# Optimization experiments

Measured on AMD Instinct MI355X. Metric: run time of the kernel, lower is better.

The kernel has to match this reference:

```python
import jax, jax.numpy as jnp
import numpy as np

EPS = 1e-5

def _ln(x, g, b):
    mu = jnp.mean(x, axis=-1, keepdims=True)
    var = jnp.mean(jnp.square(x - mu), axis=-1, keepdims=True)
    return (x - mu) * jax.lax.rsqrt(var + EPS) * g + b

def setup_inputs() -> dict:
    B, T, D, E, H, M = 2, 2048, 1024, 8, 512, 2048
    key = jax.random.key(0)
    ks = jax.random.split(key, 24)
    s = 0.02
    inp = {}
    inp['x'] = jax.random.normal(ks[0], (B, T, D), jnp.float32)
    flat = jnp.arange(M, dtype=jnp.int32) * 2  # unique token ids over B*T
    inp['index_b'] = flat // T
    inp['index_t'] = flat % T
    # shared SwiGLU (hidden = H)
    inp['sw1'] = jax.random.normal(ks[1], (H, D), jnp.float32) * s
    inp['sb1'] = jnp.zeros((H,), jnp.float32)
    inp['sw2'] = jax.random.normal(ks[2], (H, D), jnp.float32) * s
    inp['sb2'] = jnp.zeros((H,), jnp.float32)
    inp['sw3'] = jax.random.normal(ks[3], (D, H), jnp.float32) * s
    inp['sb3'] = jnp.zeros((D,), jnp.float32)
    inp['s_ln_g'] = jnp.ones((H,), jnp.float32)
    inp['s_ln_b'] = jnp.zeros((H,), jnp.float32)
    # gates
    inp['sg_w'] = jax.random.normal(ks[4], (1, D), jnp.float32) * s
    inp['sg_b'] = jnp.zeros((1,), jnp.float32)
    inp['eg_w'] = jax.random.normal(ks[5], (E, D), jnp.float32) * s
    inp['eg_b'] = jnp.zeros((E,), jnp.float32)
    inp['exp_bias'] = jnp.zeros((E,), jnp.float32)
    # per-expert SwiGLU stacks
    inp['ew1'] = jax.random.normal(ks[6], (E, H, D), jnp.float32) * s
    inp['eb1'] = jnp.zeros((E, H), jnp.float32)
    inp['ew2'] = jax.random.normal(ks[7], (E, H, D), jnp.float32) * s
    inp['eb2'] = jnp.zeros((E, H), jnp.float32)
    inp['ew3'] = jax.random.normal(ks[8], (E, D, H), jnp.float32) * s
    inp['eb3'] = jnp.zeros((E, D), jnp.float32)
    inp['sel_ln_g'] = jnp.ones((H,), jnp.float32)
    inp['sel_ln_b'] = jnp.zeros((H,), jnp.float32)
    return inp

def _forward(x, index_b, index_t, sw1, sb1, sw2, sb2, sw3, sb3, s_ln_g, s_ln_b,
             sg_w, sg_b, eg_w, eg_b, exp_bias, ew1, eb1, ew2, eb2, ew3, eb3,
             sel_ln_g, sel_ln_b):
    # shared SwiGLU over all tokens: [B,T,D]
    x1 = jnp.einsum('btd,hd->bth', x, sw1) + sb1
    x2 = jnp.einsum('btd,hd->bth', x, sw2) + sb2
    sh = _ln(jax.nn.silu(x1) * x2, s_ln_g, s_ln_b)
    shared_out = jnp.einsum('bth,dh->btd', sh, sw3) + sb3
    # MoE tokens
    x_moe = x[index_b, index_t]  # [M,D]
    shared_scores = jax.nn.sigmoid(x_moe @ sg_w.T + sg_b)       # [M,1]
    expert_scores = jax.nn.sigmoid(x_moe @ eg_w.T + eg_b)       # [M,E]
    top1_idx = jnp.argmax(expert_scores + exp_bias, axis=-1)    # [M]
    top1_score = jnp.take_along_axis(expert_scores, top1_idx[:, None], axis=-1)  # [M,1]
    weights = jax.nn.softmax(jnp.concatenate([shared_scores, top1_score], axis=-1), axis=-1)
    shared_w, expert_w = weights[:, 0], weights[:, 1]
    shared_moe_out = shared_out[index_b, index_t] * shared_w[:, None]
    # per-expert SwiGLU computed densely for all E, then token selects its expert
    h1 = jnp.einsum('md,ehd->meh', x_moe, ew1) + eb1  # [M,E,H]
    h2 = jnp.einsum('md,ehd->meh', x_moe, ew2) + eb2
    z = _ln(jax.nn.silu(h1) * h2, sel_ln_g, sel_ln_b)
    out_all = jnp.einsum('meh,edh->med', z, ew3) + eb3  # [M,E,D]
    expert_out = jnp.take_along_axis(out_all, top1_idx[:, None, None], axis=1)[:, 0]  # [M,D]
    expert_moe_out = expert_out * expert_w[:, None]
    final_out = shared_out.at[index_b, index_t].set(shared_moe_out + expert_moe_out)
    return final_out

def reference(x, index_b, index_t, sw1, sb1, sw2, sb2, sw3, sb3, s_ln_g, s_ln_b,
              sg_w, sg_b, eg_w, eg_b, exp_bias, ew1, eb1, ew2, eb2, ew3, eb3,
              sel_ln_g, sel_ln_b):
    return _forward(x, index_b, index_t, sw1, sb1, sw2, sb2, sw3, sb3, s_ln_g, s_ln_b,
                    sg_w, sg_b, eg_w, eg_b, exp_bias, ew1, eb1, ew2, eb2, ew3, eb3,
                    sel_ln_g, sel_ln_b)
```

## Files before the change

### kernel.cpp

```cpp
#include <hip/hip_runtime.h>
#include <cstdint>

typedef unsigned short u16;
typedef __bf16 bf16x8 __attribute__((ext_vector_type(8)));
typedef float f32x4 __attribute__((ext_vector_type(4)));

#define T_SEQ  2048
#define D_DIM  1024
#define H_DIM  512
#define E_NUM  8
#define M_TOK  2048
#define BT_TOK 4096
#define MAXP   3072
#define NSPLIT_NONE (1 << 28)

static __device__ __forceinline__ u16 f2bf(float f) {
    union { float f; uint32_t u; } v; v.f = f;
    uint32_t u = v.u;
    return (u16)((u + 0x7FFFu + ((u >> 16) & 1u)) >> 16);
}
static __device__ __forceinline__ uint32_t pack2(float a, float b) {
    return (uint32_t)f2bf(a) | ((uint32_t)f2bf(b) << 16);
}

static __device__ __forceinline__ void gl_lds16(const u16* g, u16* l) {
    __builtin_amdgcn_global_load_lds(
        (const __attribute__((address_space(1))) uint32_t*)g,
        (__attribute__((address_space(3))) uint32_t*)l, 16, 0, 0);
}

static __device__ __forceinline__ int find_expert(int m, const int* __restrict__ base) {
    int e = 0;
    #pragma unroll
    for (int ee = 0; ee < E_NUM - 1; ++ee)
        if (m >= base[ee + 1]) e = ee + 1;
    return e;
}


__device__ __forceinline__ void gating_body(
    int m,
    const float* __restrict__ x,
    const int* __restrict__ ib, const int* __restrict__ itx,
    const float* __restrict__ sgw, const float* __restrict__ sgb,
    const float* __restrict__ egw, const float* __restrict__ egb,
    const float* __restrict__ ebias,
    float* __restrict__ shw, float* __restrict__ expw,
    int* __restrict__ top1, int* __restrict__ rowidx,
    float* xs, float* sc)
{
    int tid = threadIdx.x;
    int row = ib[m] * T_SEQ + itx[m];
    if (tid == 0) rowidx[m] = row;
    const float* xr = x + (size_t)row * D_DIM;
    ((float4*)xs)[tid] = ((const float4*)xr)[tid];
    __syncthreads();
    int lane = tid & 63, w4 = tid >> 6;
    for (int sidx = w4; sidx < 9; sidx += 4) {
        const float* wr = (sidx == 0) ? sgw : (egw + (size_t)(sidx - 1) * D_DIM);
        float acc = 0.f;
        #pragma unroll
        for (int i = 0; i < 4; ++i) {
            int idx = i * 64 + lane;
            float4 xv = ((const float4*)xs)[idx];
            float4 wv = ((const float4*)wr)[idx];
            acc += xv.x * wv.x + xv.y * wv.y + xv.z * wv.z + xv.w * wv.w;
        }
        #pragma unroll
        for (int o = 32; o > 0; o >>= 1) acc += __shfl_xor(acc, o);
        if (lane == 0) sc[sidx] = acc;
    }
    __syncthreads();
    if (tid == 0) {
        float ss = 1.f / (1.f + expf(-(sc[0] + sgb[0])));
        float es[E_NUM];
        float best = -1e30f; int bi = 0;
        #pragma unroll
        for (int e = 0; e < E_NUM; ++e) {
            es[e] = 1.f / (1.f + expf(-(sc[1 + e] + egb[e])));
            float t = es[e] + ebias[e];
            if (t > best) { best = t; bi = e; }
        }
        float ts = es[bi];
        shw[m]  = 1.f / (1.f + expf(ts - ss));
        expw[m] = 1.f / (1.f + expf(ss - ts));
        top1[m] = bi;
    }
}

__device__ __forceinline__ void bucket_body(
    const int* __restrict__ top1,
    int* __restrict__ base, int* __restrict__ cnt, int* __restrict__ perm,
    int* sm)
{
    int* lc  = sm;
    int* lb  = sm + E_NUM;
    int* cur = sm + 2 * E_NUM + 1;
    int tid = threadIdx.x;
    if (tid < E_NUM) { lc[tid] = 0; cur[tid] = 0; }
    __syncthreads();
    for (int m = tid; m < M_TOK; m += 256) atomicAdd(&lc[top1[m]], 1);
    __syncthreads();
    if (tid == 0) {
        int bacc = 0;
        for (int e = 0; e < E_NUM; ++e) { lb[e] = bacc; bacc += (lc[e] + 127) & ~127; }
        lb[E_NUM] = bacc;
    }
    __syncthreads();
    for (int m = tid; m < M_TOK; m += 256) {
        int e = top1[m];
        int pos = lb[e] + atomicAdd(&cur[e], 1);
        perm[pos] = m;
    }
    if (tid <= E_NUM) base[tid] = lb[tid];
    if (tid < E_NUM)  cnt[tid]  = lc[tid];
}

template<bool SEL>
__device__ __forceinline__ void ln_body(
    int m,
    const float* __restrict__ X,
    const float* __restrict__ g, const float* __restrict__ b,
    u16* __restrict__ out,
    const int* __restrict__ base, const int* __restrict__ cnt,
    float* red)
{
    int tid = threadIdx.x;
    if (SEL) {
        bool valid = false;
        int tot = base[E_NUM];
        if (m < tot) {
            int e = find_expert(m, base);
            valid = (m - base[e]) < cnt[e];
        }
        if (!valid) {
            out[(size_t)m * H_DIM + tid] = 0;
            out[(size_t)m * H_DIM + tid + 256] = 0;
            return;
        }
    }
    const float* row = X + (size_t)m * D_DIM;
    float a0 = row[tid],       c0 = row[H_DIM + tid];
    float a1 = row[tid + 256], c1 = row[H_DIM + tid + 256];
    float v0 = (a0 / (1.f + expf(-a0))) * c0;
    float v1 = (a1 / (1.f + expf(-a1))) * c1;
    float s = v0 + v1, s2 = v0 * v0 + v1 * v1;
    #pragma unroll
    for (int o = 32; o > 0; o >>= 1) {
        s  += __shfl_xor(s, o);
        s2 += __shfl_xor(s2, o);
    }
    int w = tid >> 6;
    if ((tid & 63) == 0) { red[w] = s; red[4 + w] = s2; }
    __syncthreads();
    s  = red[0] + red[1] + red[2] + red[3];
    s2 = red[4] + red[5] + red[6] + red[7];
    float mu  = s * (1.f / H_DIM);
    float var = s2 * (1.f / H_DIM) - mu * mu;
    float inv = rsqrtf(var + 1e-5f);
    out[(size_t)m * H_DIM + tid]       = f2bf((v0 - mu) * inv * g[tid] + b[tid]);
    out[(size_t)m * H_DIM + tid + 256] = f2bf((v1 - mu) * inv * g[tid + 256] + b[tid + 256]);
}

template<int MODE, int KLEN>
__device__ __forceinline__ void gemm_body(
    int bn, int bm,
    const u16* __restrict__ A, int lda,
    const u16* __restrict__ W0, const u16* __restrict__ W1, int nsplit,
    const float* __restrict__ b0, const float* __restrict__ b1,
    float* __restrict__ C,
    const int* __restrict__ base, const int* __restrict__ cnt,
    const int* __restrict__ perm, const int* __restrict__ rowidx,
    const float* __restrict__ shw, const float* __restrict__ expw,
    u16* lds)
{
    constexpr int NITER = KLEN / 64;
    const int tid   = threadIdx.x;
    const int mbase = bm * 128;

    int pend = 0;
    if (MODE >= 2) {
        const int tot = base[E_NUM];
        if (mbase >= tot) return;
        int e = find_expert(mbase, base);
        pend = base[e] + cnt[e];
        if (mbase >= pend) return;
        const size_t wstride = (size_t)H_DIM * D_DIM;
        W0 += (size_t)e * wstride;
        if (MODE == 2) W1 += (size_t)e * wstride;
        b0 += e * ((MODE == 2) ? H_DIM : D_DIM);
        if (MODE == 2) b1 += e * H_DIM;
    }

    const int w  = tid >> 6;
    const int l  = tid & 63;
    const int sr = tid >> 3;
    const int sc = tid & 7;

    const u16* agp[4];
    #pragma unroll
    for (int t = 0; t < 4; ++t) {
        int r = t * 32 + sr;
        int grow;
        if (MODE == 2) {
            int p  = mbase + r;
            int pp = (p < pend) ? p : (pend - 1);
            grow = rowidx[perm[pp]];
        } else {
            grow = mbase + r;
        }
        agp[t] = A + (size_t)grow * lda + (sc ^ (r & 7)) * 8;
    }
    const u16* bgp[4];
    #pragma unroll
    for (int t = 0; t < 4; ++t) {
        int r = t * 32 + sr;
        int n = bn * 128 + r;
        bgp[t] = ((n < nsplit) ? (W0 + (size_t)n * KLEN)
                               : (W1 + (size_t)(n - nsplit) * KLEN)) + (sc ^ (r & 7)) * 8;
    }

    const int l16 = l & 15, quad = l >> 4;
    const int wm = w >> 1, wn = w & 1;

    int avo[4], bvo[4];
    #pragma unroll
    for (int i = 0; i < 4; ++i) {
        int R = wm * 64 + i * 16 + l16;
        avo[i] = R * 128 + ((quad ^ (R & 7)) * 16);
    }
    #pragma unroll
    for (int j = 0; j < 4; ++j) {
        int R = wn * 64 + j * 16 + l16;
        bvo[j] = 16384 + R * 128 + ((quad ^ (R & 7)) * 16);
    }

    f32x4 acc[4][4];
    #pragma unroll
    for (int i = 0; i < 4; ++i)
        #pragma unroll
        for (int j = 0; j < 4; ++j)
            acc[i][j] = (f32x4){0.f, 0.f, 0.f, 0.f};

    const int kstart = (bm + bn * 3) & (NITER - 1);
    const char* ldsc = (const char*)lds;

    {
        int k0 = kstart * 64;
        #pragma unroll
        for (int t = 0; t < 4; ++t)
            gl_lds16(agp[t] + k0, lds + t * 2048 + w * 512);
        #pragma unroll
        for (int t = 0; t < 4; ++t)
            gl_lds16(bgp[t] + k0, lds + 8192 + t * 2048 + w * 512);
    }
    __syncthreads();

    for (int it = 0; it < NITER; ++it) {
        const int cur = it & 1;
        if (it + 1 < NITER) {
            int k0 = ((it + 1 + kstart) & (NITER - 1)) * 64;
            u16* lb = lds + (cur ^ 1) * 16384;
            #pragma unroll
            for (int t = 0; t < 4; ++t)
                gl_lds16(agp[t] + k0, lb + t * 2048 + w * 512);
            #pragma unroll
            for (int t = 0; t < 4; ++t)
                gl_lds16(bgp[t] + k0, lb + 8192 + t * 2048 + w * 512);
        }
        const char* lb = ldsc + cur * 32768;
        #pragma unroll
        for (int kx = 0; kx < 2; ++kx) {
            bf16x8 av[4], bv[4];
            #pragma unroll
            for (int i = 0; i < 4; ++i)
                av[i] = *(const bf16x8*)(lb + (avo[i] ^ (kx * 64)));
            #pragma unroll
            for (int j = 0; j < 4; ++j)
                bv[j] = *(const bf16x8*)(lb + (bvo[j] ^ (kx * 64)));
            #pragma unroll
            for (int i = 0; i < 4; ++i)
                #pragma unroll
                for (int j = 0; j < 4; ++j)
                    acc[i][j] = __builtin_amdgcn_mfma_f32_16x16x32_bf16(av[i], bv[j], acc[i][j], 0, 0, 0);
        }
        if (it + 1 < NITER) __syncthreads();
    }

    if (MODE == 3) {
        #pragma unroll
        for (int i = 0; i < 4; ++i) {
            #pragma unroll
            for (int rr = 0; rr < 4; ++rr) {
                int p = mbase + wm * 64 + i * 16 + quad * 4 + rr;
                if (p < pend) {
                    int tok = perm[p];
                    int row = rowidx[tok];
                    float sw = shw[tok], ew = expw[tok];
                    float* outr = C + (size_t)row * D_DIM;
                    #pragma unroll
                    for (int j = 0; j < 4; ++j) {
                        int gn = bn * 128 + wn * 64 + j * 16 + l16;
                        outr[gn] = outr[gn] * sw + (acc[i][j][rr] + b0[gn]) * ew;
                    }
                }
            }
        }
    } else {
        #pragma unroll
        for (int i = 0; i < 4; ++i) {
            #pragma unroll
            for (int rr = 0; rr < 4; ++rr) {
                int gm = mbase + wm * 64 + i * 16 + quad * 4 + rr;
                float* outr = C + (size_t)gm * D_DIM;
                #pragma unroll
                for (int j = 0; j < 4; ++j) {
                    int gn = bn * 128 + wn * 64 + j * 16 + l16;
                    float bias = (gn < nsplit) ? b0[gn] : b1[gn - nsplit];
                    outr[gn] = acc[i][j][rr] + bias;
                }
            }
        }
    }
}


__global__ __launch_bounds__(256)
void k_cvt_gating(const float* __restrict__ x,
                  const float* __restrict__ sw1, const float* __restrict__ sw2,
                  const float* __restrict__ sw3,
                  const float* __restrict__ ew1, const float* __restrict__ ew2,
                  const float* __restrict__ ew3,
                  u16* __restrict__ xb,
                  u16* __restrict__ sw1b, u16* __restrict__ sw2b, u16* __restrict__ sw3b,
                  u16* __restrict__ ew1b, u16* __restrict__ ew2b, u16* __restrict__ ew3b,
                  const int* __restrict__ ib, const int* __restrict__ itx,
                  const float* __restrict__ sgw, const float* __restrict__ sgb,
                  const float* __restrict__ egw, const float* __restrict__ egb,
                  const float* __restrict__ ebias,
                  float* __restrict__ shw, float* __restrict__ expw,
                  int* __restrict__ top1, int* __restrict__ rowidx)
{
    __shared__ __align__(16) float smem[D_DIM + 16];
    int bx = blockIdx.x;
    if (bx >= 17920) {
        gating_body(bx - 17920, x, ib, itx, sgw, sgb, egw, egb, ebias,
                    shw, expw, top1, rowidx, smem, smem + D_DIM);
        return;
    }
    long i = (long)bx * 256 + threadIdx.x;
    const float* s; u16* d; long off;
    if      (i < 1048576) { s = x;   d = xb;   off = i; }
    else if (i < 1179648) { s = sw1; d = sw1b; off = i - 1048576; }
    else if (i < 1310720) { s = sw2; d = sw2b; off = i - 1179648; }
    else if (i < 1441792) { s = sw3; d = sw3b; off = i - 1310720; }
    else if (i < 2490368) { s = ew1; d = ew1b; off = i - 1441792; }
    else if (i < 3538944) { s = ew2; d = ew2b; off = i - 2490368; }
    else                  { s = ew3; d = ew3b; off = i - 3538944; }
    float4 v = ((const float4*)s)[off];
    uint2 o;
    o.x = pack2(v.x, v.y);
    o.y = pack2(v.z, v.w);
    ((uint2*)d)[off] = o;
}

__global__ __launch_bounds__(256)
void k_g1_bucket(const u16* __restrict__ xb,
                 const u16* __restrict__ sw1b, const u16* __restrict__ sw2b,
                 const float* __restrict__ sb1, const float* __restrict__ sb2,
                 float* __restrict__ x12,
                 const int* __restrict__ top1,
                 int* __restrict__ basep, int* __restrict__ cntp, int* __restrict__ perm)
{
    __shared__ __align__(16) u16 lds[2 * (128 + 128) * 64];
    int bx = blockIdx.x;
    if (bx < 256) {
        gemm_body<0, 1024>(bx & 7, bx >> 3, xb, D_DIM, sw1b, sw2b, H_DIM, sb1, sb2, x12,
                           nullptr, nullptr, nullptr, nullptr, nullptr, nullptr, lds);
    } else {
        bucket_body(top1, basep, cntp, perm, (int*)lds);
    }
}

__global__ __launch_bounds__(256)
void k_ln(const float* __restrict__ x12,
          const float* __restrict__ g, const float* __restrict__ b,
          u16* __restrict__ shn)
{
    __shared__ __align__(16) float smf[8];
    ln_body<false>(blockIdx.x, x12, g, b, shn, nullptr, nullptr, smf);
}

__global__ __launch_bounds__(256)
void k_g2_e1(const u16* __restrict__ shn, const u16* __restrict__ sw3b,
             const float* __restrict__ sb3, float* __restrict__ out,
             const u16* __restrict__ xb,
             const u16* __restrict__ ew1b, const u16* __restrict__ ew2b,
             const float* __restrict__ eb1, const float* __restrict__ eb2,
             float* __restrict__ h12,
             const int* __restrict__ basep, const int* __restrict__ cntp,
             const int* __restrict__ perm, const int* __restrict__ rowidx)
{
    __shared__ __align__(16) u16 lds[2 * (128 + 128) * 64];
    int bx = blockIdx.x;
    if (bx < 256) {
        gemm_body<1, 512>(bx & 7, bx >> 3, shn, H_DIM, sw3b, sw3b, NSPLIT_NONE, sb3, sb3, out,
                          nullptr, nullptr, nullptr, nullptr, nullptr, nullptr, lds);
    } else {
        int b2 = bx - 256;
        gemm_body<2, 1024>(b2 & 7, b2 >> 3, xb, D_DIM, ew1b, ew2b, H_DIM, eb1, eb2, h12,
                           basep, cntp, perm, rowidx, nullptr, nullptr, lds);
    }
}

__global__ __launch_bounds__(256)
void k_ln_sel(const float* __restrict__ h12,
              const float* __restrict__ g, const float* __restrict__ b,
              u16* __restrict__ z,
              const int* __restrict__ basep, const int* __restrict__ cntp)
{
    __shared__ __align__(16) float smf[8];
    ln_body<true>(blockIdx.x, h12, g, b, z, basep, cntp, smf);
}

__global__ __launch_bounds__(256)
void k_e2(const u16* __restrict__ z, const u16* __restrict__ ew3b,
          const float* __restrict__ eb3, float* __restrict__ out,
          const int* __restrict__ basep, const int* __restrict__ cntp,
          const int* __restrict__ perm, const int* __restrict__ rowidx,
          const float* __restrict__ shw, const float* __restrict__ expw)
{
    __shared__ __align__(16) u16 lds[2 * (128 + 128) * 64];
    int bx = blockIdx.x;
    gemm_body<3, 512>(bx & 7, bx >> 3, z, H_DIM, ew3b, ew3b, NSPLIT_NONE, eb3, eb3, out,
                      basep, cntp, perm, rowidx, shw, expw, lds);
}

extern "C" void kernel_launch(void* const* d_in, const int* in_sizes, int n_in,
                              void* d_out, int out_size, void* d_ws, size_t ws_size,
                              hipStream_t stream) {
    const float* x        = (const float*)d_in[0];
    const int*   index_b  = (const int*)d_in[1];
    const int*   index_t  = (const int*)d_in[2];
    const float* sw1      = (const float*)d_in[3];
    const float* sb1      = (const float*)d_in[4];
    const float* sw2      = (const float*)d_in[5];
    const float* sb2      = (const float*)d_in[6];
    const float* sw3      = (const float*)d_in[7];
    const float* sb3      = (const float*)d_in[8];
    const float* s_ln_g   = (const float*)d_in[9];
    const float* s_ln_b   = (const float*)d_in[10];
    const float* sg_w     = (const float*)d_in[11];
    const float* sg_b     = (const float*)d_in[12];
    const float* eg_w     = (const float*)d_in[13];
    const float* eg_b     = (const float*)d_in[14];
    const float* exp_bias = (const float*)d_in[15];
    const float* ew1      = (const float*)d_in[16];
    const float* eb1      = (const float*)d_in[17];
    const float* ew2      = (const float*)d_in[18];
    const float* eb2      = (const float*)d_in[19];
    const float* ew3      = (const float*)d_in[20];
    const float* eb3      = (const float*)d_in[21];
    const float* sel_ln_g = (const float*)d_in[22];
    const float* sel_ln_b = (const float*)d_in[23];
    float* out = (float*)d_out;
    char*  ws  = (char*)d_ws;

    u16*   xb   = (u16*)(ws + 0);
    u16*   sw1b = (u16*)(ws + 8388608);
    u16*   sw2b = (u16*)(ws + 9437184);
    u16*   sw3b = (u16*)(ws + 10485760);
    u16*   ew1b = (u16*)(ws + 11534336);
    u16*   ew2b = (u16*)(ws + 19922944);
    u16*   ew3b = (u16*)(ws + 28311552);
    float* x12  = (float*)(ws + 36700160);
    float* h12  = x12;
    u16*   sh   = (u16*)(ws + 53477376);
    u16*   z    = sh;
    float* shw    = (float*)(ws + 57671680);
    float* expw   = shw + M_TOK;
    int*   top1   = (int*)(expw + M_TOK);
    int*   rowidx = top1 + M_TOK;
    int*   perm   = rowidx + M_TOK;
    int*   basep  = perm + MAXP;
    int*   cntp   = basep + 16;

    k_cvt_gating<<<dim3(17920 + M_TOK), dim3(256), 0, stream>>>(
        x, sw1, sw2, sw3, ew1, ew2, ew3,
        xb, sw1b, sw2b, sw3b, ew1b, ew2b, ew3b,
        index_b, index_t, sg_w, sg_b, eg_w, eg_b, exp_bias,
        shw, expw, top1, rowidx);

    k_g1_bucket<<<dim3(256 + 1), dim3(256), 0, stream>>>(
        xb, sw1b, sw2b, sb1, sb2, x12, top1, basep, cntp, perm);

    k_ln<<<dim3(BT_TOK), dim3(256), 0, stream>>>(x12, s_ln_g, s_ln_b, sh);

    k_g2_e1<<<dim3(256 + 8 * (MAXP / 128)), dim3(256), 0, stream>>>(
        sh, sw3b, sb3, out,
        xb, ew1b, ew2b, eb1, eb2, h12,
        basep, cntp, perm, rowidx);

    k_ln_sel<<<dim3(MAXP), dim3(256), 0, stream>>>(
        h12, sel_ln_g, sel_ln_b, z, basep, cntp);

    k_e2<<<dim3(8 * (MAXP / 128)), dim3(256), 0, stream>>>(
        z, ew3b, eb3, out, basep, cntp, perm, rowidx, shw, expw);
}
```

Before: 228.4 us.

## Rebalance kernel schedule to overlap weight conversion, layernorms and GEMMs

Only x, sw1 and sw2 are converted to bf16 before the first GEMM. The remaining weight conversions (sw3, ew1, ew2, ew3) now run in the same launch as the first GEMM and bucketing. The shared layernorm moves into the expert-up GEMM launch, and the selected-expert layernorm moves into the shared-down GEMM launch, removing one launch. h12 and z get separate workspace buffers so these co-scheduled stages no longer alias. The aim is to overlap bandwidth-bound conversion and layernorm work with GEMMs and cut serialization, at the cost of more workspace and possible contention between co-resident blocks.

```diff
diff --git a/kernel.cpp b/kernel.cpp
--- a/kernel.cpp
+++ b/kernel.cpp
@@ -35,6 +35,15 @@
     for (int ee = 0; ee < E_NUM - 1; ++ee)
         if (m >= base[ee + 1]) e = ee + 1;
     return e;
+}
+
+static __device__ __forceinline__ void cvt4(const float* __restrict__ s,
+                                            u16* __restrict__ d, long off) {
+    float4 v = ((const float4*)s)[off];
+    uint2 o;
+    o.x = pack2(v.x, v.y);
+    o.y = pack2(v.z, v.w);
+    ((uint2*)d)[off] = o;
 }
 
 
@@ -326,74 +335,63 @@
 
 
 __global__ __launch_bounds__(256)
-void k_cvt_gating(const float* __restrict__ x,
-                  const float* __restrict__ sw1, const float* __restrict__ sw2,
-                  const float* __restrict__ sw3,
-                  const float* __restrict__ ew1, const float* __restrict__ ew2,
-                  const float* __restrict__ ew3,
-                  u16* __restrict__ xb,
-                  u16* __restrict__ sw1b, u16* __restrict__ sw2b, u16* __restrict__ sw3b,
-                  u16* __restrict__ ew1b, u16* __restrict__ ew2b, u16* __restrict__ ew3b,
-                  const int* __restrict__ ib, const int* __restrict__ itx,
-                  const float* __restrict__ sgw, const float* __restrict__ sgb,
-                  const float* __restrict__ egw, const float* __restrict__ egb,
-                  const float* __restrict__ ebias,
-                  float* __restrict__ shw, float* __restrict__ expw,
-                  int* __restrict__ top1, int* __restrict__ rowidx)
+void k_cvt1_gating(const float* __restrict__ x,
+                   const float* __restrict__ sw1, const float* __restrict__ sw2,
+                   u16* __restrict__ xb, u16* __restrict__ sw1b, u16* __restrict__ sw2b,
+                   const int* __restrict__ ib, const int* __restrict__ itx,
+                   const float* __restrict__ sgw, const float* __restrict__ sgb,
+                   const float* __restrict__ egw, const float* __restrict__ egb,
+                   const float* __restrict__ ebias,
+                   float* __restrict__ shw, float* __restrict__ expw,
+                   int* __restrict__ top1, int* __restrict__ rowidx)
 {
     __shared__ __align__(16) float smem[D_DIM + 16];
     int bx = blockIdx.x;
-    if (bx >= 17920) {
-        gating_body(bx - 17920, x, ib, itx, sgw, sgb, egw, egb, ebias,
+    if (bx >= 5120) {
+        gating_body(bx - 5120, x, ib, itx, sgw, sgb, egw, egb, ebias,
                     shw, expw, top1, rowidx, smem, smem + D_DIM);
         return;
     }
     long i = (long)bx * 256 + threadIdx.x;
-    const float* s; u16* d; long off;
-    if      (i < 1048576) { s = x;   d = xb;   off = i; }
-    else if (i < 1179648) { s = sw1; d = sw1b; off = i - 1048576; }
-    else if (i < 1310720) { s = sw2; d = sw2b; off = i - 1179648; }
-    else if (i < 1441792) { s = sw3; d = sw3b; off = i - 1310720; }
-    else if (i < 2490368) { s = ew1; d = ew1b; off = i - 1441792; }
-    else if (i < 3538944) { s = ew2; d = ew2b; off = i - 2490368; }
-    else                  { s = ew3; d = ew3b; off = i - 3538944; }
-    float4 v = ((const float4*)s)[off];
-    uint2 o;
-    o.x = pack2(v.x, v.y);
-    o.y = pack2(v.z, v.w);
-    ((uint2*)d)[off] = o;
+    if      (i < 1048576) cvt4(x,   xb,   i);
+    else if (i < 1179648) cvt4(sw1, sw1b, i - 1048576);
+    else                  cvt4(sw2, sw2b, i - 1179648);
 }
 
 __global__ __launch_bounds__(256)
-void k_g1_bucket(const u16* __restrict__ xb,
-                 const u16* __restrict__ sw1b, const u16* __restrict__ sw2b,
-                 const float* __restrict__ sb1, const float* __restrict__ sb2,
-                 float* __restrict__ x12,
-                 const int* __restrict__ top1,
-                 int* __restrict__ basep, int* __restrict__ cntp, int* __restrict__ perm)
+void k_g1_bucket_cvt2(const u16* __restrict__ xb,
+                      const u16* __restrict__ sw1b, const u16* __restrict__ sw2b,
+                      const float* __restrict__ sb1, const float* __restrict__ sb2,
+                      float* __restrict__ x12,
+                      const int* __restrict__ top1,
+                      int* __restrict__ basep, int* __restrict__ cntp, int* __restrict__ perm,
+                      const float* __restrict__ sw3, const float* __restrict__ ew1,
+                      const float* __restrict__ ew2, const float* __restrict__ ew3,
+                      u16* __restrict__ sw3b, u16* __restrict__ ew1b,
+                      u16* __restrict__ ew2b, u16* __restrict__ ew3b)
 {
     __shared__ __align__(16) u16 lds[2 * (128 + 128) * 64];
     int bx = blockIdx.x;
     if (bx < 256) {
         gemm_body<0, 1024>(bx & 7, bx >> 3, xb, D_DIM, sw1b, sw2b, H_DIM, sb1, sb2, x12,
                            nullptr, nullptr, nullptr, nullptr, nullptr, nullptr, lds);
-    } else {
+        return;
+    }
+    if (bx == 256) {
         bucket_body(top1, basep, cntp, perm, (int*)lds);
-    }
+        return;
+    }
+    long i = (long)(bx - 257) * 256 + threadIdx.x;
+    if      (i <  131072) cvt4(sw3, sw3b, i);
+    else if (i < 1179648) cvt4(ew1, ew1b, i - 131072);
+    else if (i < 2228224) cvt4(ew2, ew2b, i - 1179648);
+    else                  cvt4(ew3, ew3b, i - 2228224);
 }
 
 __global__ __launch_bounds__(256)
-void k_ln(const float* __restrict__ x12,
-          const float* __restrict__ g, const float* __restrict__ b,
-          u16* __restrict__ shn)
-{
-    __shared__ __align__(16) float smf[8];
-    ln_body<false>(blockIdx.x, x12, g, b, shn, nullptr, nullptr, smf);
-}
-
-__global__ __launch_bounds__(256)
-void k_g2_e1(const u16* __restrict__ shn, const u16* __restrict__ sw3b,
-             const float* __restrict__ sb3, float* __restrict__ out,
+void k_ln_e1(const float* __restrict__ x12,
+             const float* __restrict__ g, const float* __restrict__ b,
+             u16* __restrict__ shn,
              const u16* __restrict__ xb,
              const u16* __restrict__ ew1b, const u16* __restrict__ ew2b,
              const float* __restrict__ eb1, const float* __restrict__ eb2,
@@ -403,24 +401,31 @@
 {
     __shared__ __align__(16) u16 lds[2 * (128 + 128) * 64];
     int bx = blockIdx.x;
+    if (bx < BT_TOK) {
+        ln_body<false>(bx, x12, g, b, shn, nullptr, nullptr, (float*)lds);
+    } else {
+        int b2 = bx - BT_TOK;
+        gemm_body<2, 1024>(b2 & 7, b2 >> 3, xb, D_DIM, ew1b, ew2b, H_DIM, eb1, eb2, h12,
+                           basep, cntp, perm, rowidx, nullptr, nullptr, lds);
+    }
+}
+
+__global__ __launch_bounds__(256)
+void k_g2_lnsel(const u16* __restrict__ shn, const u16* __restrict__ sw3b,
+                const float* __restrict__ sb3, float* __restrict__ out,
+                const float* __restrict__ h12,
+                const float* __restrict__ selg, const float* __restrict__ selb,
+                u16* __restrict__ z,
+                const int* __restrict__ basep, const int* __restrict__ cntp)
+{
+    __shared__ __align__(16) u16 lds[2 * (128 + 128) * 64];
+    int bx = blockIdx.x;
     if (bx < 256) {
         gemm_body<1, 512>(bx & 7, bx >> 3, shn, H_DIM, sw3b, sw3b, NSPLIT_NONE, sb3, sb3, out,
                           nullptr, nullptr, nullptr, nullptr, nullptr, nullptr, lds);
     } else {
-        int b2 = bx - 256;
-        gemm_body<2, 1024>(b2 & 7, b2 >> 3, xb, D_DIM, ew1b, ew2b, H_DIM, eb1, eb2, h12,
-                           basep, cntp, perm, rowidx, nullptr, nullptr, lds);
-    }
-}
-
-__global__ __launch_bounds__(256)
-void k_ln_sel(const float* __restrict__ h12,
-              const float* __restrict__ g, const float* __restrict__ b,
-              u16* __restrict__ z,
-              const int* __restrict__ basep, const int* __restrict__ cntp)
-{
-    __shared__ __align__(16) float smf[8];
-    ln_body<true>(blockIdx.x, h12, g, b, z, basep, cntp, smf);
+        ln_body<true>(bx - 256, h12, selg, selb, z, basep, cntp, (float*)lds);
+    }
 }
 
 __global__ __launch_bounds__(256)
@@ -474,9 +479,7 @@
     u16*   ew2b = (u16*)(ws + 19922944);
     u16*   ew3b = (u16*)(ws + 28311552);
     float* x12  = (float*)(ws + 36700160);
-    float* h12  = x12;
     u16*   sh   = (u16*)(ws + 53477376);
-    u16*   z    = sh;
     float* shw    = (float*)(ws + 57671680);
     float* expw   = shw + M_TOK;
     int*   top1   = (int*)(expw + M_TOK);
@@ -484,24 +487,25 @@
     int*   perm   = rowidx + M_TOK;
     int*   basep  = perm + MAXP;
     int*   cntp   = basep + 16;
-
-    k_cvt_gating<<<dim3(17920 + M_TOK), dim3(256), 0, stream>>>(
-        x, sw1, sw2, sw3, ew1, ew2, ew3,
-        xb, sw1b, sw2b, sw3b, ew1b, ew2b, ew3b,
+    float* h12  = (float*)(ws + 58720256);
+    u16*   z    = (u16*)(ws + 71303168);
+
+    k_cvt1_gating<<<dim3(5120 + M_TOK), dim3(256), 0, stream>>>(
+        x, sw1, sw2, xb, sw1b, sw2b,
         index_b, index_t, sg_w, sg_b, eg_w, eg_b, exp_bias,
         shw, expw, top1, rowidx);
 
-    k_g1_bucket<<<dim3(256 + 1), dim3(256), 0, stream>>>(
-        xb, sw1b, sw2b, sb1, sb2, x12, top1, basep, cntp, perm);
-
-    k_ln<<<dim3(BT_TOK), dim3(256), 0, stream>>>(x12, s_ln_g, s_ln_b, sh);
-
-    k_g2_e1<<<dim3(256 + 8 * (MAXP / 128)), dim3(256), 0, stream>>>(
-        sh, sw3b, sb3, out,
+    k_g1_bucket_cvt2<<<dim3(257 + 12800), dim3(256), 0, stream>>>(
+        xb, sw1b, sw2b, sb1, sb2, x12, top1, basep, cntp, perm,
+        sw3, ew1, ew2, ew3, sw3b, ew1b, ew2b, ew3b);
+
+    k_ln_e1<<<dim3(BT_TOK + 8 * (MAXP / 128)), dim3(256), 0, stream>>>(
+        x12, s_ln_g, s_ln_b, sh,
         xb, ew1b, ew2b, eb1, eb2, h12,
         basep, cntp, perm, rowidx);
 
-    k_ln_sel<<<dim3(MAXP), dim3(256), 0, stream>>>(
+    k_g2_lnsel<<<dim3(256 + MAXP), dim3(256), 0, stream>>>(
+        sh, sw3b, sb3, out,
         h12, sel_ln_g, sel_ln_b, z, basep, cntp);
 
     k_e2<<<dim3(8 * (MAXP / 128)), dim3(256), 0, stream>>>(
```

Measured after the change: 251.9 us. 1.1x slower.
